# Performance work log

Hardware: AMD Instinct MI355X
Metric: run time of the kernel (lower is better)

## Reference

```python
import jax, jax.numpy as jnp
import numpy as np
from jax import lax

HEADS = 8

def rotate_every_two(x):
    x1 = x[..., ::2]
    x2 = x[..., 1::2]
    return jnp.stack([-x2, x1], axis=-1).reshape(x.shape)

def theta_shift(x, sin, cos):
    # x: (b,n,N,d); sin/cos: (N,d) broadcast over b,n
    return x * cos + rotate_every_two(x) * sin

def setup_inputs() -> dict:
    key = jax.random.key(0)
    ks = jax.random.split(key, 8)
    B, C, H, W = 8, 256, 64, 64
    hd = C // HEADS
    return {
        'x': jax.random.normal(ks[0], (B, C, H, W), jnp.float32),
        'sin': jax.random.normal(ks[1], (H * W, hd), jnp.float32),
        'cos': jax.random.normal(ks[2], (H * W, hd), jnp.float32),
        'w_qkvo': jax.random.normal(ks[3], (4 * C, C), jnp.float32) * 0.02,
        'b_qkvo': jnp.zeros((4 * C,), jnp.float32),
        'w_lepe': jax.random.normal(ks[4], (C, 1, 5, 5), jnp.float32) * 0.02,
        'b_lepe': jnp.zeros((C,), jnp.float32),
        'w_proj': jax.random.normal(ks[5], (C, C), jnp.float32) * 0.02,
        'b_proj': jnp.zeros((C,), jnp.float32),
    }

def reference(x, sin, cos, w_qkvo, b_qkvo, w_lepe, b_lepe, w_proj, b_proj):
    B, C, H, W = x.shape
    heads = HEADS
    hd = C // heads
    N = H * W
    scale = hd ** (-0.5)

    # 1x1 conv qkvo
    qkvo = jnp.einsum('bchw,oc->bohw', x, w_qkvo) + b_qkvo[None, :, None, None]
    qkv = qkvo[:, :3 * C]
    o = qkvo[:, 3 * C:]

    # depthwise 5x5 lepe on v channels
    v_img = qkv[:, 2 * C:]
    lepe = lax.conv_general_dilated(
        v_img, w_lepe, (1, 1), [(2, 2), (2, 2)],
        dimension_numbers=('NCHW', 'OIHW', 'NCHW'),
        feature_group_count=C) + b_lepe[None, :, None, None]

    # b (m n d) h w -> m b n (h w) d
    qkv_r = qkv.reshape(B, 3, heads, hd, N).transpose(1, 0, 2, 4, 3)
    q, k, v = qkv_r[0], qkv_r[1], qkv_r[2]  # (b,n,N,d)

    q = jax.nn.elu(q) + 1.0
    k = jax.nn.elu(k) + 1.0

    # z = q @ mean_k^T * scale -> (b,n,N,1)
    z = jnp.einsum('bnld,bnd->bnl', q, k.mean(axis=2))[..., None] * scale

    q = theta_shift(q, sin, cos)
    k = theta_shift(k, sin, cos)

    s = (scale / N) ** 0.5
    kv = jnp.einsum('bnld,bnle->bnde', k * s, v * s)  # (b,n,d,d)
    v_mean = v.mean(axis=2, keepdims=True)  # (b,n,1,d)

    res = jnp.einsum('bnld,bnde->bnle', q, kv) * (1.0 + 1.0 / (z + 1e-6)) - z * v_mean

    # b n (h w) d -> b (n d) h w
    res = res.transpose(0, 1, 3, 2).reshape(B, C, H, W)
    res = res + lepe

    out = jnp.einsum('bchw,oc->bohw', res * o, w_proj) + b_proj[None, :, None, None]
    return out
```

## Files before the change

### kernel.cpp

```cpp
#include <hip/hip_runtime.h>
#include <hip/hip_bf16.h>

typedef unsigned short u16;
typedef unsigned int u32;
typedef short bf16x8 __attribute__((ext_vector_type(8)));
typedef float f32x4 __attribute__((ext_vector_type(4)));
typedef u32 u32x4 __attribute__((ext_vector_type(4)));

#define N_TOK 4096
#define C_DIM 256
#define HEADS 8
#define HD 32
#define SCALE_F 0.17677669529663687f

__device__ inline u16 f2bf(float f) {
    u32 u = __float_as_uint(f);
    u += 0x7fffu + ((u >> 16) & 1u);
    return (u16)(u >> 16);
}
__device__ inline float b2f(u16 h) { return __uint_as_float((u32)h << 16); }
__device__ inline float bf_lo(u32 u) { return __uint_as_float(u << 16); }
__device__ inline float bf_hi(u32 u) { return __uint_as_float(u & 0xffff0000u); }

__device__ inline void gload16(const void* g, void* l) {
    __builtin_amdgcn_global_load_lds((const __attribute__((address_space(1))) u32*)g,
                                     (__attribute__((address_space(3))) u32*)l, 16, 0, 0);
}

__global__ __launch_bounds__(256) void stage1(const float* __restrict__ x, const float* __restrict__ w1,
                                              const float* __restrict__ w2, const float* __restrict__ s,
                                              const float* __restrict__ c, u16* __restrict__ xT,
                                              u16* __restrict__ o1, u16* __restrict__ o2, u32* __restrict__ scT) {
    __shared__ char smem[16896];
    int bx = blockIdx.x;
    int t = threadIdx.x;
    if (bx < 2048) {
        int lt = bx & 63, ct = (bx >> 6) & 3, b = bx >> 8;
        int l0 = lt * 64, c0 = ct * 64;
        const float* xb = x + ((size_t)b * C_DIM + c0) * N_TOK + l0;
        float* tl = (float*)smem;
#pragma unroll
        for (int i = 0; i < 4; ++i) {
            int id = i * 256 + t;
            int ci = id >> 4, lj = id & 15;
            f32x4 v = *(const f32x4*)(xb + (size_t)ci * N_TOK + lj * 4);
#pragma unroll
            for (int e = 0; e < 4; ++e) tl[(lj * 4 + e) * 65 + ci] = v[e];
        }
        __syncthreads();
#pragma unroll
        for (int j = 0; j < 2; ++j) {
            int id = j * 256 + t;
            int l = id >> 3, cg = id & 7;
            u16 o[8];
#pragma unroll
            for (int e = 0; e < 8; ++e) o[e] = f2bf(tl[l * 65 + cg * 8 + e]);
            uint4 u;
            u.x = (u32)o[0] | ((u32)o[1] << 16);
            u.y = (u32)o[2] | ((u32)o[3] << 16);
            u.z = (u32)o[4] | ((u32)o[5] << 16);
            u.w = (u32)o[6] | ((u32)o[7] << 16);
            *(uint4*)(xT + ((size_t)b * N_TOK + l0 + l) * C_DIM + c0 + cg * 8) = u;
        }
        return;
    }
    int px = bx - 2048;
    if (px < 1024) {
        int i = px * 256 + t;
        o1[i] = f2bf(w1[i]);
        if (i < 256 * 256) o2[i] = f2bf(w2[i]);
        return;
    }
    int l0 = (px - 1024) * 64;
    float (*ts)[33] = (float(*)[33])smem;
    float (*tc)[33] = (float(*)[33])(smem + 8448);
    int d = t & 31, r = t >> 5;
#pragma unroll
    for (int i = 0; i < 8; ++i) {
        ts[r + i * 8][d] = s[(size_t)(l0 + r + i * 8) * HD + d];
        tc[r + i * 8][d] = c[(size_t)(l0 + r + i * 8) * HD + d];
    }
    __syncthreads();
    int li = t & 63, dr = t >> 6;
#pragma unroll
    for (int i = 0; i < 8; ++i) {
        int dd = dr * 8 + i;
        scT[(size_t)dd * N_TOK + l0 + li] = (u32)f2bf(ts[li][dd]) | ((u32)f2bf(tc[li][dd]) << 16);
    }
}

__global__ __launch_bounds__(256) void gemm_proj(const u16* __restrict__ A, const u16* __restrict__ Bm,
                                                 const float* __restrict__ bias, float* __restrict__ C,
                                                 int M, int L, int K) {
    int bt = blockIdx.z;
    int m0 = blockIdx.y * 128;
    int l0 = blockIdx.x * 128;
    const u16* Bb = Bm + (size_t)bt * L * K;
    float* Cb = C + (size_t)bt * M * L;

    __shared__ u16 smem[17408];
    u16* As = smem;
    u16* Bs = smem + 8192;

    int t = threadIdx.x;
    int w = t >> 6, lane = t & 63;
    int wr = (w >> 1) * 64, wc = (w & 1) * 64;
    int fr = lane & 15, kg = lane >> 4;

    f32x4 acc[4][4] = {};

    for (int k0 = 0; k0 < K; k0 += 64) {
#pragma unroll
        for (int j = 0; j < 4; ++j) {
            int c = j * 256 + w * 64 + lane;
            int row = c >> 3, slot = c & 7;
            int gslot = slot ^ (row & 7);
            u16* abase = As + (size_t)(j * 256 + w * 64) * 8;
            u16* bbase = Bs + (size_t)(j * 256 + w * 64) * 8;
            gload16(A + (size_t)(m0 + row) * K + k0 + gslot * 8, abase);
            gload16(Bb + (size_t)(l0 + row) * K + k0 + gslot * 8, bbase);
        }
        __syncthreads();
#pragma unroll
        for (int kk = 0; kk < 2; ++kk) {
            bf16x8 af[4], bfr[4];
#pragma unroll
            for (int i = 0; i < 4; ++i) {
                int ra = wr + i * 16 + fr;
                int rb = wc + i * 16 + fr;
                af[i]  = *(const bf16x8*)(As + (size_t)ra * 64 + (size_t)((kk * 4 + kg) ^ (ra & 7)) * 8);
                bfr[i] = *(const bf16x8*)(Bs + (size_t)rb * 64 + (size_t)((kk * 4 + kg) ^ (rb & 7)) * 8);
            }
#pragma unroll
            for (int i = 0; i < 4; ++i)
#pragma unroll
                for (int jj = 0; jj < 4; ++jj)
                    acc[i][jj] = __builtin_amdgcn_mfma_f32_16x16x32_bf16(af[i], bfr[jj], acc[i][jj], 0, 0, 0);
        }
        __syncthreads();
    }

    int rg = (lane >> 4) * 4;
    float* Csf = (float*)smem;
#pragma unroll
    for (int half = 0; half < 2; ++half) {
        if ((w >> 1) == half) {
#pragma unroll
            for (int i = 0; i < 4; ++i)
#pragma unroll
                for (int jj = 0; jj < 4; ++jj) {
                    int col = wc + jj * 16 + fr;
#pragma unroll
                    for (int r = 0; r < 4; ++r) {
                        int row = i * 16 + rg + r;
                        Csf[row * 132 + col] = acc[i][jj][r] + bias[m0 + half * 64 + row];
                    }
                }
        }
        __syncthreads();
#pragma unroll
        for (int j = 0; j < 8; ++j) {
            int id = j * 256 + t;
            int row = id >> 5, c4 = id & 31;
            *(f32x4*)(Cb + (size_t)(m0 + half * 64 + row) * L + l0 + c4 * 4) =
                *(const f32x4*)(Csf + row * 132 + c4 * 4);
        }
        __syncthreads();
    }
}

__global__ __launch_bounds__(256) void stage2_kv(const u16* __restrict__ wbf, const float* __restrict__ bq,
                                                 const u16* __restrict__ xT, const u32* __restrict__ scT,
                                                 u16* __restrict__ v_glob, float* __restrict__ part_kv,
                                                 float* __restrict__ part_ks, float* __restrict__ part_vs) {
    int chunk = blockIdx.x & 15, bn = blockIdx.x >> 4;
    int b = bn >> 3, n = bn & 7;
    int T0 = chunk * 256;
    const u16* Bx = xT + ((size_t)b * N_TOK + T0) * C_DIM;

    __shared__ char smem[51200];
    u16* Bst = (u16*)smem;
    u16* Ast = (u16*)(smem + 32768);
    u16 (*ks_bf)[264] = (u16(*)[264])smem;
    u16 (*v_bf)[264]  = (u16(*)[264])(smem + 16896);
    float* red  = (float*)(smem + 33792);
    float* redk = (float*)(smem + 50176);
    float* redv = (float*)(smem + 50688);

    int t = threadIdx.x;
    int w = t >> 6, lane = t & 63;
    int fr = lane & 15, kg = lane >> 4;

    float bk[8], bv[8];
#pragma unroll
    for (int i = 0; i < 2; ++i)
#pragma unroll
        for (int r = 0; r < 4; ++r) {
            bk[i * 4 + r] = bq[256 + n * HD + i * 16 + kg * 4 + r];
            bv[i * 4 + r] = bq[512 + n * HD + i * 16 + kg * 4 + r];
        }

    f32x4 acc[4][4] = {};
    for (int k0 = 0; k0 < 256; k0 += 64) {
#pragma unroll
        for (int j = 0; j < 8; ++j) {
            int c = j * 256 + w * 64 + lane;
            int row = c >> 3, slot = c & 7;
            int gslot = slot ^ (row & 7);
            gload16(Bx + (size_t)row * C_DIM + k0 + gslot * 8, Bst + (size_t)(j * 256 + w * 64) * 8);
        }
#pragma unroll
        for (int j = 0; j < 2; ++j) {
            int c = j * 256 + w * 64 + lane;
            int row = c >> 3, slot = c & 7;
            int gslot = slot ^ (row & 7);
            int arow = (row < 32 ? 256 : 480) + n * HD + row;
            gload16(wbf + (size_t)arow * C_DIM + k0 + gslot * 8, Ast + (size_t)(j * 256 + w * 64) * 8);
        }
        __syncthreads();
#pragma unroll
        for (int kk = 0; kk < 2; ++kk) {
            bf16x8 af[4], bfr[4];
#pragma unroll
            for (int i = 0; i < 4; ++i) {
                int ra = i * 16 + fr;
                af[i] = *(const bf16x8*)(Ast + (size_t)ra * 64 + (size_t)((kk * 4 + kg) ^ (ra & 7)) * 8);
            }
#pragma unroll
            for (int jj = 0; jj < 4; ++jj) {
                int rb = w * 64 + jj * 16 + fr;
                bfr[jj] = *(const bf16x8*)(Bst + (size_t)rb * 64 + (size_t)((kk * 4 + kg) ^ (rb & 7)) * 8);
            }
#pragma unroll
            for (int i = 0; i < 4; ++i)
#pragma unroll
                for (int jj = 0; jj < 4; ++jj)
                    acc[i][jj] = __builtin_amdgcn_mfma_f32_16x16x32_bf16(af[i], bfr[jj], acc[i][jj], 0, 0, 0);
        }
        __syncthreads();
    }

    float kspart[8] = {}, vspart[8] = {};
#pragma unroll
    for (int i = 0; i < 2; ++i)
#pragma unroll
        for (int jj = 0; jj < 4; ++jj) {
            int tok = w * 64 + jj * 16 + fr;
            float k0v = acc[i][jj][0] + bk[i * 4 + 0];
            float k1v = acc[i][jj][1] + bk[i * 4 + 1];
            float k2v = acc[i][jj][2] + bk[i * 4 + 2];
            float k3v = acc[i][jj][3] + bk[i * 4 + 3];
            float e0 = k0v > 0.f ? k0v + 1.f : __expf(k0v);
            float e1 = k1v > 0.f ? k1v + 1.f : __expf(k1v);
            float e2 = k2v > 0.f ? k2v + 1.f : __expf(k2v);
            float e3 = k3v > 0.f ? k3v + 1.f : __expf(k3v);
            kspart[i * 4 + 0] += e0; kspart[i * 4 + 1] += e1;
            kspart[i * 4 + 2] += e2; kspart[i * 4 + 3] += e3;
            int d0 = i * 16 + kg * 4;
            u32 sA = scT[(size_t)(d0 + 0) * N_TOK + T0 + tok];
            u32 sB = scT[(size_t)(d0 + 1) * N_TOK + T0 + tok];
            u32 sC = scT[(size_t)(d0 + 2) * N_TOK + T0 + tok];
            u32 sD = scT[(size_t)(d0 + 3) * N_TOK + T0 + tok];
            ks_bf[d0 + 0][tok] = f2bf(e0 * bf_hi(sA) - e1 * bf_lo(sA));
            ks_bf[d0 + 1][tok] = f2bf(e1 * bf_hi(sB) + e0 * bf_lo(sB));
            ks_bf[d0 + 2][tok] = f2bf(e2 * bf_hi(sC) - e3 * bf_lo(sC));
            ks_bf[d0 + 3][tok] = f2bf(e3 * bf_hi(sD) + e2 * bf_lo(sD));
        }
#pragma unroll
    for (int i = 2; i < 4; ++i)
#pragma unroll
        for (int jj = 0; jj < 4; ++jj) {
            int tok = w * 64 + jj * 16 + fr;
#pragma unroll
            for (int r = 0; r < 4; ++r) {
                int vrow = (i - 2) * 16 + kg * 4 + r;
                float vv_ = acc[i][jj][r] + bv[(i - 2) * 4 + r];
                vspart[(i - 2) * 4 + r] += vv_;
                v_bf[vrow][tok] = f2bf(vv_);
            }
        }
#pragma unroll
    for (int m = 1; m < 16; m <<= 1) {
#pragma unroll
        for (int q = 0; q < 8; ++q) {
            kspart[q] += __shfl_xor(kspart[q], m);
            vspart[q] += __shfl_xor(vspart[q], m);
        }
    }
    if (fr == 0) {
#pragma unroll
        for (int q = 0; q < 8; ++q) {
            int row = (q >> 2) * 16 + kg * 4 + (q & 3);
            redk[w * 32 + row] = kspart[q];
            redv[w * 32 + row] = vspart[q];
        }
    }
    __syncthreads();

    f32x4 a2[2][2] = {};
#pragma unroll
    for (int kc = 0; kc < 2; ++kc) {
        int kcol = w * 64 + kc * 32 + kg * 8;
        bf16x8 af[2], bfv[2];
#pragma unroll
        for (int i = 0; i < 2; ++i) {
            af[i]  = *(const bf16x8*)&ks_bf[i * 16 + fr][kcol];
            bfv[i] = *(const bf16x8*)&v_bf[i * 16 + fr][kcol];
        }
#pragma unroll
        for (int i = 0; i < 2; ++i)
#pragma unroll
            for (int jj = 0; jj < 2; ++jj)
                a2[i][jj] = __builtin_amdgcn_mfma_f32_16x16x32_bf16(af[i], bfv[jj], a2[i][jj], 0, 0, 0);
    }

    {
        int row = t >> 3, tg = t & 7;
        u16* vg = v_glob + ((size_t)(b * C_DIM + n * HD + row)) * N_TOK + T0 + tg * 32;
#pragma unroll
        for (int q = 0; q < 4; ++q)
            *(uint4*)(vg + q * 8) = *(const uint4*)&v_bf[row][tg * 32 + q * 8];
    }
    if (t < 32) {
        float s = redk[t] + redk[32 + t] + redk[64 + t] + redk[96 + t];
        float sv = redv[t] + redv[32 + t] + redv[64 + t] + redv[96 + t];
        part_ks[((size_t)bn * 16 + chunk) * 32 + t] = s;
        part_vs[((size_t)bn * 16 + chunk) * 32 + t] = sv;
    }

#pragma unroll
    for (int i = 0; i < 2; ++i)
#pragma unroll
        for (int jj = 0; jj < 2; ++jj)
#pragma unroll
            for (int r = 0; r < 4; ++r) {
                int row = i * 16 + kg * 4 + r;
                int col = jj * 16 + fr;
                red[w * 1024 + row * 32 + col] = a2[i][jj][r];
            }
    __syncthreads();
    float* pkv = part_kv + ((size_t)bn * 16 + chunk) * 1024;
#pragma unroll
    for (int i = 0; i < 4; ++i) {
        int el = i * 256 + t;
        pkv[el] = red[el] + red[1024 + el] + red[2048 + el] + red[3072 + el];
    }
}

__global__ __launch_bounds__(256) void kvfinal_lepe(const float* __restrict__ part_kv, const float* __restrict__ part_ks,
                                                    const float* __restrict__ part_vs, const u16* __restrict__ v_glob,
                                                    const float* __restrict__ wl, const float* __restrict__ bl,
                                                    u16* __restrict__ kvT_bf, float* __restrict__ kmean,
                                                    float* __restrict__ vmean, u16* __restrict__ lepe) {
    __shared__ float wc5[25];
    int bx = blockIdx.x;
    int t = threadIdx.x;
    if (bx < 64) {
        int bn = bx;
        const float* p = part_kv + (size_t)bn * 16 * 1024;
        const float s2c = SCALE_F / (float)N_TOK;
#pragma unroll
        for (int i = 0; i < 4; ++i) {
            int sl = t + i * 256;
            float s = 0;
#pragma unroll
            for (int c = 0; c < 16; ++c) s += p[(size_t)c * 1024 + sl];
            float val = s * s2c;
            int d = sl >> 5, e = sl & 31;
            kvT_bf[(size_t)bn * 1024 + e * 32 + d] = f2bf(val);
        }
        if (t < 32) {
            float s = 0, sv = 0;
            for (int c = 0; c < 16; ++c) {
                s  += part_ks[((size_t)bn * 16 + c) * 32 + t];
                sv += part_vs[((size_t)bn * 16 + c) * 32 + t];
            }
            kmean[bn * 32 + t] = s * (1.f / (float)N_TOK);
            vmean[bn * 32 + t] = sv * (1.f / (float)N_TOK);
        }
        return;
    }
    int i2 = bx - 64;
    int c = i2 & 255, b = i2 >> 8;
    const u16* src = v_glob + ((size_t)(b * C_DIM + c)) * N_TOK;
    u16* dst = lepe + ((size_t)b * C_DIM + c) * N_TOK;
    if (t < 25) wc5[t] = wl[c * 25 + t];
    __syncthreads();

    int h = t >> 2, w0 = (t & 3) * 16;
    float bb = bl[c];
    float o16[16];
#pragma unroll
    for (int i = 0; i < 16; ++i) o16[i] = bb;

#pragma unroll
    for (int dh = 0; dh < 5; ++dh) {
        int gr = h + dh - 2;
        bool rowok = (gr >= 0) && (gr < 64);
        const u16* rp = src + (size_t)(rowok ? gr : 0) * 64 + w0 - 8;
        bf16x8 L0 = ((const bf16x8*)rp)[0];
        bf16x8 L1 = ((const bf16x8*)rp)[1];
        bf16x8 L2 = ((const bf16x8*)rp)[2];
        bf16x8 L3 = ((const bf16x8*)rp)[3];
        float rbuf[32];
#pragma unroll
        for (int j = 0; j < 32; ++j) {
            int col = w0 - 8 + j;
            u16 raw = (u16)(j < 8 ? L0[j] : j < 16 ? L1[j - 8] : j < 24 ? L2[j - 16] : L3[j - 24]);
            bool ok = rowok && (col >= 0) && (col < 64);
            rbuf[j] = ok ? b2f(raw) : 0.f;
        }
#pragma unroll
        for (int dw = 0; dw < 5; ++dw) {
            float wv_ = wc5[dh * 5 + dw];
#pragma unroll
            for (int ow = 0; ow < 16; ++ow)
                o16[ow] += rbuf[6 + dw + ow] * wv_;
        }
    }

    uint4 u0, u1;
    u0.x = (u32)f2bf(o16[0]) | ((u32)f2bf(o16[1]) << 16);
    u0.y = (u32)f2bf(o16[2]) | ((u32)f2bf(o16[3]) << 16);
    u0.z = (u32)f2bf(o16[4]) | ((u32)f2bf(o16[5]) << 16);
    u0.w = (u32)f2bf(o16[6]) | ((u32)f2bf(o16[7]) << 16);
    u1.x = (u32)f2bf(o16[8]) | ((u32)f2bf(o16[9]) << 16);
    u1.y = (u32)f2bf(o16[10]) | ((u32)f2bf(o16[11]) << 16);
    u1.z = (u32)f2bf(o16[12]) | ((u32)f2bf(o16[13]) << 16);
    u1.w = (u32)f2bf(o16[14]) | ((u32)f2bf(o16[15]) << 16);
    *(uint4*)(dst + h * 64 + w0) = u0;
    *(uint4*)(dst + h * 64 + w0 + 8) = u1;
}

__global__ __launch_bounds__(256) void attn_epilogue(const u16* __restrict__ wbf, const float* __restrict__ bq,
                                                     const u16* __restrict__ xT, const u32* __restrict__ scT,
                                                     const u16* __restrict__ kvT_bf, const float* __restrict__ kmean,
                                                     const float* __restrict__ vmean, const u16* __restrict__ lepe,
                                                     u16* __restrict__ resnT) {
    int lt = blockIdx.x, bn = blockIdx.y;
    int b = bn >> 3, n = bn & 7;
    int T0 = lt * 256;
    const u16* lp = lepe + ((size_t)b * C_DIM + n * HD) * N_TOK;
    const u16* Bx = xT + ((size_t)b * N_TOK + T0) * C_DIM;

    __shared__ char smem[64256];
    u16* qA    = (u16*)smem;
    u16* o_lds = (u16*)(smem + 20480);
    u16* Rt    = (u16*)(smem + 40960);
    u16* kvb   = (u16*)(smem + 61440);
    float* kml = (float*)(smem + 64000);
    float* vml = (float*)(smem + 64128);
    u16* Bst = (u16*)smem;
    u16* Ast = (u16*)(smem + 32768);

    int t = threadIdx.x;
    int w = t >> 6, lane = t & 63;
    int fr = lane & 15, kg = lane >> 4;

    if (t < 128) {
        int e = t >> 2, d0 = (t & 3) * 8;
        *(uint4*)(kvb + e * 40 + d0) = *(const uint4*)(kvT_bf + (size_t)bn * 1024 + e * 32 + d0);
    }
    if (t < 32) { kml[t] = kmean[bn * 32 + t]; vml[t] = vmean[bn * 32 + t]; }

    f32x4 acc[4][4] = {};
    for (int k0 = 0; k0 < 256; k0 += 64) {
#pragma unroll
        for (int j = 0; j < 8; ++j) {
            int c = j * 256 + w * 64 + lane;
            int row = c >> 3, slot = c & 7;
            int gslot = slot ^ (row & 7);
            gload16(Bx + (size_t)row * C_DIM + k0 + gslot * 8, Bst + (size_t)(j * 256 + w * 64) * 8);
        }
#pragma unroll
        for (int j = 0; j < 2; ++j) {
            int c = j * 256 + w * 64 + lane;
            int row = c >> 3, slot = c & 7;
            int gslot = slot ^ (row & 7);
            int arow = (row < 32 ? n * HD : 736 + n * HD) + row;
            gload16(wbf + (size_t)arow * C_DIM + k0 + gslot * 8, Ast + (size_t)(j * 256 + w * 64) * 8);
        }
        __syncthreads();
#pragma unroll
        for (int kk = 0; kk < 2; ++kk) {
            bf16x8 af[4], bfr[4];
#pragma unroll
            for (int i = 0; i < 4; ++i) {
                int ra = i * 16 + fr;
                af[i] = *(const bf16x8*)(Ast + (size_t)ra * 64 + (size_t)((kk * 4 + kg) ^ (ra & 7)) * 8);
            }
#pragma unroll
            for (int jj = 0; jj < 4; ++jj) {
                int rb = w * 64 + jj * 16 + fr;
                bfr[jj] = *(const bf16x8*)(Bst + (size_t)rb * 64 + (size_t)((kk * 4 + kg) ^ (rb & 7)) * 8);
            }
#pragma unroll
            for (int i = 0; i < 4; ++i)
#pragma unroll
                for (int jj = 0; jj < 4; ++jj)
                    acc[i][jj] = __builtin_amdgcn_mfma_f32_16x16x32_bf16(af[i], bfr[jj], acc[i][jj], 0, 0, 0);
        }
        __syncthreads();
    }
    int rg = kg * 4;
#pragma unroll
    for (int i = 0; i < 4; ++i)
#pragma unroll
        for (int jj = 0; jj < 4; ++jj) {
            int tok = w * 64 + jj * 16 + fr;
#pragma unroll
            for (int r = 0; r < 4; ++r) {
                int qorow = i * 16 + rg + r;
                int brow = (qorow < 32 ? n * HD : 736 + n * HD) + qorow;
                u16 val = f2bf(acc[i][jj][r] + bq[brow]);
                if (qorow < 32) qA[tok * 40 + qorow] = val;
                else            o_lds[tok * 40 + qorow - 32] = val;
            }
        }
    __syncthreads();

    int token = T0 + t;
    float qv[32];
    float z = 0.f;
#pragma unroll
    for (int j = 0; j < 4; ++j) {
        bf16x8 q8 = *(const bf16x8*)(qA + t * 40 + j * 8);
#pragma unroll
        for (int e = 0; e < 8; ++e) {
            float x_ = b2f((u16)q8[e]);
            float e_ = x_ > 0.f ? x_ + 1.f : __expf(x_);
            qv[j * 8 + e] = e_;
            z += e_ * kml[j * 8 + e];
        }
    }
    z *= SCALE_F;
#pragma unroll
    for (int p = 0; p < 16; ++p) {
        u32 sc0 = scT[(size_t)(2 * p) * N_TOK + token];
        u32 sc1 = scT[(size_t)(2 * p + 1) * N_TOK + token];
        float se = bf_lo(sc0), ce = bf_hi(sc0);
        float so = bf_lo(sc1), co = bf_hi(sc1);
        float a = qv[2 * p], bb = qv[2 * p + 1];
        qv[2 * p]     = a * ce - bb * se;
        qv[2 * p + 1] = bb * co + a * so;
    }
    float mult = 1.f + 1.f / (z + 1e-6f);
#pragma unroll
    for (int j4 = 0; j4 < 4; ++j4) {
        uint4 u;
        u.x = (u32)f2bf(qv[8 * j4 + 0]) | ((u32)f2bf(qv[8 * j4 + 1]) << 16);
        u.y = (u32)f2bf(qv[8 * j4 + 2]) | ((u32)f2bf(qv[8 * j4 + 3]) << 16);
        u.z = (u32)f2bf(qv[8 * j4 + 4]) | ((u32)f2bf(qv[8 * j4 + 5]) << 16);
        u.w = (u32)f2bf(qv[8 * j4 + 6]) | ((u32)f2bf(qv[8 * j4 + 7]) << 16);
        *(uint4*)(qA + t * 40 + j4 * 8) = u;
    }
    __syncthreads();

    {
        bf16x8 af[4], bfr[2];
#pragma unroll
        for (int i = 0; i < 4; ++i)
            af[i] = *(const bf16x8*)(qA + (size_t)(w * 64 + i * 16 + fr) * 40 + kg * 8);
#pragma unroll
        for (int jj = 0; jj < 2; ++jj)
            bfr[jj] = *(const bf16x8*)(kvb + (jj * 16 + fr) * 40 + kg * 8);

        u16* Rw = Rt + w * 2560;
        f32x4 zero = {0.f, 0.f, 0.f, 0.f};
#pragma unroll
        for (int i = 0; i < 4; ++i)
#pragma unroll
            for (int jj = 0; jj < 2; ++jj) {
                f32x4 a2 = __builtin_amdgcn_mfma_f32_16x16x32_bf16(af[i], bfr[jj], zero, 0, 0, 0);
#pragma unroll
                for (int r = 0; r < 4; ++r)
                    Rw[(i * 16 + kg * 4 + r) * 40 + jj * 16 + fr] = f2bf(a2[r]);
            }
    }
    __syncthreads();

    float res[32], ovv[32];
#pragma unroll
    for (int j = 0; j < 4; ++j) {
        bf16x8 r8 = *(const bf16x8*)(Rt + w * 2560 + lane * 40 + j * 8);
        bf16x8 o8 = *(const bf16x8*)(o_lds + t * 40 + j * 8);
#pragma unroll
        for (int e = 0; e < 8; ++e) {
            res[j * 8 + e] = b2f((u16)r8[e]);
            ovv[j * 8 + e] = b2f((u16)o8[e]);
        }
    }

    u16* dst0 = resnT + ((size_t)b * N_TOK + token) * C_DIM + n * HD;
#pragma unroll
    for (int g = 0; g < 4; ++g) {
        float vv[8];
#pragma unroll
        for (int e2 = 0; e2 < 8; ++e2) {
            int ee = g * 8 + e2;
            float lx = b2f(lp[(size_t)ee * N_TOK + token]);
            float rx = res[ee] * mult - z * vml[ee];
            vv[e2] = (rx + lx) * ovv[ee];
        }
        uint4 u;
        u.x = (u32)f2bf(vv[0]) | ((u32)f2bf(vv[1]) << 16);
        u.y = (u32)f2bf(vv[2]) | ((u32)f2bf(vv[3]) << 16);
        u.z = (u32)f2bf(vv[4]) | ((u32)f2bf(vv[5]) << 16);
        u.w = (u32)f2bf(vv[6]) | ((u32)f2bf(vv[7]) << 16);
        ((uint4*)(dst0 + g * 8))[0] = u;
    }
}

extern "C" void kernel_launch(void* const* d_in, const int* in_sizes, int n_in,
                              void* d_out, int out_size, void* d_ws, size_t ws_size,
                              hipStream_t stream) {
    const float* x      = (const float*)d_in[0];
    const float* sinp   = (const float*)d_in[1];
    const float* cosp   = (const float*)d_in[2];
    const float* w_qkvo = (const float*)d_in[3];
    const float* b_qkvo = (const float*)d_in[4];
    const float* w_lepe = (const float*)d_in[5];
    const float* b_lepe = (const float*)d_in[6];
    const float* w_proj = (const float*)d_in[7];
    const float* b_proj = (const float*)d_in[8];

    char* ws = (char*)d_ws;
    size_t off = 0;
    auto alloc = [&](size_t bytes) { size_t o = off; off = (off + bytes + 255) & ~(size_t)255; return o; };
    u16*   wbf     = (u16*)(ws + alloc((size_t)1024 * 256 * 2));
    u16*   wpbf    = (u16*)(ws + alloc((size_t)256 * 256 * 2));
    u16*   xT      = (u16*)(ws + alloc((size_t)8 * 4096 * 256 * 2));
    u16*   v_glob  = (u16*)(ws + alloc((size_t)8 * 256 * 4096 * 2));
    u16*   lepe    = (u16*)(ws + alloc((size_t)8 * 256 * 4096 * 2));
    u16*   resnT   = (u16*)(ws + alloc((size_t)8 * 4096 * 256 * 2));
    float* part_kv = (float*)(ws + alloc((size_t)64 * 16 * 1024 * 4));
    float* part_ks = (float*)(ws + alloc((size_t)64 * 16 * 32 * 4));
    float* part_vs = (float*)(ws + alloc((size_t)64 * 16 * 32 * 4));
    u16*   kvT_bf  = (u16*)(ws + alloc((size_t)64 * 1024 * 2));
    float* kmean   = (float*)(ws + alloc((size_t)64 * 32 * 4));
    float* vmean   = (float*)(ws + alloc((size_t)64 * 32 * 4));
    u32*   scT     = (u32*)(ws + alloc((size_t)32 * 4096 * 4));
    if (off > ws_size) return;

    stage1<<<dim3(3136), dim3(256), 0, stream>>>(x, w_qkvo, w_proj, sinp, cosp, xT, wbf, wpbf, scT);
    stage2_kv<<<dim3(1024), dim3(256), 0, stream>>>(wbf, b_qkvo, xT, scT, v_glob, part_kv, part_ks, part_vs);
    kvfinal_lepe<<<dim3(2112), dim3(256), 0, stream>>>(part_kv, part_ks, part_vs, v_glob, w_lepe, b_lepe,
                                                       kvT_bf, kmean, vmean, lepe);
    attn_epilogue<<<dim3(16, 64), dim3(256), 0, stream>>>(wbf, b_qkvo, xT, scT, kvT_bf, kmean, vmean, lepe, resnT);
    gemm_proj<<<dim3(32, 2, 8), dim3(256), 0, stream>>>(wpbf, resnT, b_proj, (float*)d_out, 256, 4096, 256);
}
```

Measured before the change: 92.75 us.

## Double-buffer LDS staging in stage2_kv and attn_epilogue GEMM loops

Both projection GEMM loops now use two LDS buffers, so the global-to-LDS loads for the next K-slice are issued before the MFMAs on the current slice run. This hides memory latency behind compute. In attn_epilogue the loads of kv, kmean and vmean move after the GEMM, since the enlarged staging area overlaps their LDS region. The cost is LDS growing to 80 KB per block, which can lower the number of resident blocks per CU.

```diff
diff --git a/kernel.cpp b/kernel.cpp
--- a/kernel.cpp
+++ b/kernel.cpp
@@ -178,9 +178,7 @@
     int T0 = chunk * 256;
     const u16* Bx = xT + ((size_t)b * N_TOK + T0) * C_DIM;
 
-    __shared__ char smem[51200];
-    u16* Bst = (u16*)smem;
-    u16* Ast = (u16*)(smem + 32768);
+    __shared__ char smem[81920];
     u16 (*ks_bf)[264] = (u16(*)[264])smem;
     u16 (*v_bf)[264]  = (u16(*)[264])(smem + 16896);
     float* red  = (float*)(smem + 33792);
@@ -200,36 +198,45 @@
             bv[i * 4 + r] = bq[512 + n * HD + i * 16 + kg * 4 + r];
         }
 
-    f32x4 acc[4][4] = {};
-    for (int k0 = 0; k0 < 256; k0 += 64) {
+    auto STAGE = [&](int buf, int k0) {
+        u16* Bd = (u16*)smem + buf * 16384;
+        u16* Ad = (u16*)(smem + 65536) + buf * 4096;
 #pragma unroll
         for (int j = 0; j < 8; ++j) {
-            int c = j * 256 + w * 64 + lane;
-            int row = c >> 3, slot = c & 7;
+            int cc = j * 256 + w * 64 + lane;
+            int row = cc >> 3, slot = cc & 7;
             int gslot = slot ^ (row & 7);
-            gload16(Bx + (size_t)row * C_DIM + k0 + gslot * 8, Bst + (size_t)(j * 256 + w * 64) * 8);
+            gload16(Bx + (size_t)row * C_DIM + k0 + gslot * 8, Bd + (size_t)(j * 256 + w * 64) * 8);
         }
 #pragma unroll
         for (int j = 0; j < 2; ++j) {
-            int c = j * 256 + w * 64 + lane;
-            int row = c >> 3, slot = c & 7;
+            int cc = j * 256 + w * 64 + lane;
+            int row = cc >> 3, slot = cc & 7;
             int gslot = slot ^ (row & 7);
             int arow = (row < 32 ? 256 : 480) + n * HD + row;
-            gload16(wbf + (size_t)arow * C_DIM + k0 + gslot * 8, Ast + (size_t)(j * 256 + w * 64) * 8);
-        }
-        __syncthreads();
+            gload16(wbf + (size_t)arow * C_DIM + k0 + gslot * 8, Ad + (size_t)(j * 256 + w * 64) * 8);
+        }
+    };
+
+    f32x4 acc[4][4] = {};
+    STAGE(0, 0);
+    __syncthreads();
+    for (int step = 0; step < 4; ++step) {
+        if (step < 3) STAGE((step + 1) & 1, (step + 1) * 64);
+        u16* Bc = (u16*)smem + (step & 1) * 16384;
+        u16* Ac = (u16*)(smem + 65536) + (step & 1) * 4096;
 #pragma unroll
         for (int kk = 0; kk < 2; ++kk) {
             bf16x8 af[4], bfr[4];
 #pragma unroll
             for (int i = 0; i < 4; ++i) {
                 int ra = i * 16 + fr;
-                af[i] = *(const bf16x8*)(Ast + (size_t)ra * 64 + (size_t)((kk * 4 + kg) ^ (ra & 7)) * 8);
+                af[i] = *(const bf16x8*)(Ac + (size_t)ra * 64 + (size_t)((kk * 4 + kg) ^ (ra & 7)) * 8);
             }
 #pragma unroll
             for (int jj = 0; jj < 4; ++jj) {
                 int rb = w * 64 + jj * 16 + fr;
-                bfr[jj] = *(const bf16x8*)(Bst + (size_t)rb * 64 + (size_t)((kk * 4 + kg) ^ (rb & 7)) * 8);
+                bfr[jj] = *(const bf16x8*)(Bc + (size_t)rb * 64 + (size_t)((kk * 4 + kg) ^ (rb & 7)) * 8);
             }
 #pragma unroll
             for (int i = 0; i < 4; ++i)
@@ -443,65 +450,72 @@
     const u16* lp = lepe + ((size_t)b * C_DIM + n * HD) * N_TOK;
     const u16* Bx = xT + ((size_t)b * N_TOK + T0) * C_DIM;
 
-    __shared__ char smem[64256];
+    __shared__ char smem[81920];
     u16* qA    = (u16*)smem;
     u16* o_lds = (u16*)(smem + 20480);
     u16* Rt    = (u16*)(smem + 40960);
     u16* kvb   = (u16*)(smem + 61440);
     float* kml = (float*)(smem + 64000);
     float* vml = (float*)(smem + 64128);
-    u16* Bst = (u16*)smem;
-    u16* Ast = (u16*)(smem + 32768);
 
     int t = threadIdx.x;
     int w = t >> 6, lane = t & 63;
     int fr = lane & 15, kg = lane >> 4;
 
+    auto STAGE = [&](int buf, int k0) {
+        u16* Bd = (u16*)smem + buf * 16384;
+        u16* Ad = (u16*)(smem + 65536) + buf * 4096;
+#pragma unroll
+        for (int j = 0; j < 8; ++j) {
+            int cc = j * 256 + w * 64 + lane;
+            int row = cc >> 3, slot = cc & 7;
+            int gslot = slot ^ (row & 7);
+            gload16(Bx + (size_t)row * C_DIM + k0 + gslot * 8, Bd + (size_t)(j * 256 + w * 64) * 8);
+        }
+#pragma unroll
+        for (int j = 0; j < 2; ++j) {
+            int cc = j * 256 + w * 64 + lane;
+            int row = cc >> 3, slot = cc & 7;
+            int gslot = slot ^ (row & 7);
+            int arow = (row < 32 ? n * HD : 736 + n * HD) + row;
+            gload16(wbf + (size_t)arow * C_DIM + k0 + gslot * 8, Ad + (size_t)(j * 256 + w * 64) * 8);
+        }
+    };
+
+    f32x4 acc[4][4] = {};
+    STAGE(0, 0);
+    __syncthreads();
+    for (int step = 0; step < 4; ++step) {
+        if (step < 3) STAGE((step + 1) & 1, (step + 1) * 64);
+        u16* Bc = (u16*)smem + (step & 1) * 16384;
+        u16* Ac = (u16*)(smem + 65536) + (step & 1) * 4096;
+#pragma unroll
+        for (int kk = 0; kk < 2; ++kk) {
+            bf16x8 af[4], bfr[4];
+#pragma unroll
+            for (int i = 0; i < 4; ++i) {
+                int ra = i * 16 + fr;
+                af[i] = *(const bf16x8*)(Ac + (size_t)ra * 64 + (size_t)((kk * 4 + kg) ^ (ra & 7)) * 8);
+            }
+#pragma unroll
+            for (int jj = 0; jj < 4; ++jj) {
+                int rb = w * 64 + jj * 16 + fr;
+                bfr[jj] = *(const bf16x8*)(Bc + (size_t)rb * 64 + (size_t)((kk * 4 + kg) ^ (rb & 7)) * 8);
+            }
+#pragma unroll
+            for (int i = 0; i < 4; ++i)
+#pragma unroll
+                for (int jj = 0; jj < 4; ++jj)
+                    acc[i][jj] = __builtin_amdgcn_mfma_f32_16x16x32_bf16(af[i], bfr[jj], acc[i][jj], 0, 0, 0);
+        }
+        __syncthreads();
+    }
+
     if (t < 128) {
         int e = t >> 2, d0 = (t & 3) * 8;
         *(uint4*)(kvb + e * 40 + d0) = *(const uint4*)(kvT_bf + (size_t)bn * 1024 + e * 32 + d0);
     }
     if (t < 32) { kml[t] = kmean[bn * 32 + t]; vml[t] = vmean[bn * 32 + t]; }
-
-    f32x4 acc[4][4] = {};
-    for (int k0 = 0; k0 < 256; k0 += 64) {
-#pragma unroll
-        for (int j = 0; j < 8; ++j) {
-            int c = j * 256 + w * 64 + lane;
-            int row = c >> 3, slot = c & 7;
-            int gslot = slot ^ (row & 7);
-            gload16(Bx + (size_t)row * C_DIM + k0 + gslot * 8, Bst + (size_t)(j * 256 + w * 64) * 8);
-        }
-#pragma unroll
-        for (int j = 0; j < 2; ++j) {
-            int c = j * 256 + w * 64 + lane;
-            int row = c >> 3, slot = c & 7;
-            int gslot = slot ^ (row & 7);
-            int arow = (row < 32 ? n * HD : 736 + n * HD) + row;
-            gload16(wbf + (size_t)arow * C_DIM + k0 + gslot * 8, Ast + (size_t)(j * 256 + w * 64) * 8);
-        }
-        __syncthreads();
-#pragma unroll
-        for (int kk = 0; kk < 2; ++kk) {
-            bf16x8 af[4], bfr[4];
-#pragma unroll
-            for (int i = 0; i < 4; ++i) {
-                int ra = i * 16 + fr;
-                af[i] = *(const bf16x8*)(Ast + (size_t)ra * 64 + (size_t)((kk * 4 + kg) ^ (ra & 7)) * 8);
-            }
-#pragma unroll
-            for (int jj = 0; jj < 4; ++jj) {
-                int rb = w * 64 + jj * 16 + fr;
-                bfr[jj] = *(const bf16x8*)(Bst + (size_t)rb * 64 + (size_t)((kk * 4 + kg) ^ (rb & 7)) * 8);
-            }
-#pragma unroll
-            for (int i = 0; i < 4; ++i)
-#pragma unroll
-                for (int jj = 0; jj < 4; ++jj)
-                    acc[i][jj] = __builtin_amdgcn_mfma_f32_16x16x32_bf16(af[i], bfr[jj], acc[i][jj], 0, 0, 0);
-        }
-        __syncthreads();
-    }
     int rg = kg * 4;
 #pragma unroll
     for (int i = 0; i < 4; ++i)
```

Result: slower. 95.29 us (+2.7%).

## Fuse depthwise lepe conv into attention epilogue via LDS tile

Applied to the files above, without the earlier changes.

Moves the 5x5 depthwise lepe convolution out of the separate kv-final kernel and into attn_epilogue. Each block computes the lepe values for its 4-row token tile and 32 head channels into shared memory. This removes the global lepe buffer write and re-read and leaves kv_final as a tiny 64-block kernel. In exchange, LDS use per block grows to about 80KB, which may lower occupancy, and the conv work now sits on the epilogue's critical path instead of running in parallel blocks.

```diff
diff --git a/kernel.cpp b/kernel.cpp
--- a/kernel.cpp
+++ b/kernel.cpp
@@ -204,15 +204,15 @@
     for (int k0 = 0; k0 < 256; k0 += 64) {
 #pragma unroll
         for (int j = 0; j < 8; ++j) {
-            int c = j * 256 + w * 64 + lane;
-            int row = c >> 3, slot = c & 7;
+            int cc = j * 256 + w * 64 + lane;
+            int row = cc >> 3, slot = cc & 7;
             int gslot = slot ^ (row & 7);
             gload16(Bx + (size_t)row * C_DIM + k0 + gslot * 8, Bst + (size_t)(j * 256 + w * 64) * 8);
         }
 #pragma unroll
         for (int j = 0; j < 2; ++j) {
-            int c = j * 256 + w * 64 + lane;
-            int row = c >> 3, slot = c & 7;
+            int cc = j * 256 + w * 64 + lane;
+            int row = cc >> 3, slot = cc & 7;
             int gslot = slot ^ (row & 7);
             int arow = (row < 32 ? 256 : 480) + n * HD + row;
             gload16(wbf + (size_t)arow * C_DIM + k0 + gslot * 8, Ast + (size_t)(j * 256 + w * 64) * 8);
@@ -347,109 +347,53 @@
     }
 }
 
-__global__ __launch_bounds__(256) void kvfinal_lepe(const float* __restrict__ part_kv, const float* __restrict__ part_ks,
-                                                    const float* __restrict__ part_vs, const u16* __restrict__ v_glob,
-                                                    const float* __restrict__ wl, const float* __restrict__ bl,
-                                                    u16* __restrict__ kvT_bf, float* __restrict__ kmean,
-                                                    float* __restrict__ vmean, u16* __restrict__ lepe) {
-    __shared__ float wc5[25];
-    int bx = blockIdx.x;
+__global__ __launch_bounds__(256) void kv_final(const float* __restrict__ part_kv, const float* __restrict__ part_ks,
+                                                const float* __restrict__ part_vs, u16* __restrict__ kvT_bf,
+                                                float* __restrict__ kmean, float* __restrict__ vmean) {
+    int bn = blockIdx.x;
     int t = threadIdx.x;
-    if (bx < 64) {
-        int bn = bx;
-        const float* p = part_kv + (size_t)bn * 16 * 1024;
-        const float s2c = SCALE_F / (float)N_TOK;
-#pragma unroll
-        for (int i = 0; i < 4; ++i) {
-            int sl = t + i * 256;
-            float s = 0;
-#pragma unroll
-            for (int c = 0; c < 16; ++c) s += p[(size_t)c * 1024 + sl];
-            float val = s * s2c;
-            int d = sl >> 5, e = sl & 31;
-            kvT_bf[(size_t)bn * 1024 + e * 32 + d] = f2bf(val);
-        }
-        if (t < 32) {
-            float s = 0, sv = 0;
-            for (int c = 0; c < 16; ++c) {
-                s  += part_ks[((size_t)bn * 16 + c) * 32 + t];
-                sv += part_vs[((size_t)bn * 16 + c) * 32 + t];
-            }
-            kmean[bn * 32 + t] = s * (1.f / (float)N_TOK);
-            vmean[bn * 32 + t] = sv * (1.f / (float)N_TOK);
-        }
-        return;
-    }
-    int i2 = bx - 64;
-    int c = i2 & 255, b = i2 >> 8;
-    const u16* src = v_glob + ((size_t)(b * C_DIM + c)) * N_TOK;
-    u16* dst = lepe + ((size_t)b * C_DIM + c) * N_TOK;
-    if (t < 25) wc5[t] = wl[c * 25 + t];
-    __syncthreads();
-
-    int h = t >> 2, w0 = (t & 3) * 16;
-    float bb = bl[c];
-    float o16[16];
-#pragma unroll
-    for (int i = 0; i < 16; ++i) o16[i] = bb;
-
-#pragma unroll
-    for (int dh = 0; dh < 5; ++dh) {
-        int gr = h + dh - 2;
-        bool rowok = (gr >= 0) && (gr < 64);
-        const u16* rp = src + (size_t)(rowok ? gr : 0) * 64 + w0 - 8;
-        bf16x8 L0 = ((const bf16x8*)rp)[0];
-        bf16x8 L1 = ((const bf16x8*)rp)[1];
-        bf16x8 L2 = ((const bf16x8*)rp)[2];
-        bf16x8 L3 = ((const bf16x8*)rp)[3];
-        float rbuf[32];
-#pragma unroll
-        for (int j = 0; j < 32; ++j) {
-            int col = w0 - 8 + j;
-            u16 raw = (u16)(j < 8 ? L0[j] : j < 16 ? L1[j - 8] : j < 24 ? L2[j - 16] : L3[j - 24]);
-            bool ok = rowok && (col >= 0) && (col < 64);
-            rbuf[j] = ok ? b2f(raw) : 0.f;
-        }
-#pragma unroll
-        for (int dw = 0; dw < 5; ++dw) {
-            float wv_ = wc5[dh * 5 + dw];
-#pragma unroll
-            for (int ow = 0; ow < 16; ++ow)
-                o16[ow] += rbuf[6 + dw + ow] * wv_;
-        }
-    }
-
-    uint4 u0, u1;
-    u0.x = (u32)f2bf(o16[0]) | ((u32)f2bf(o16[1]) << 16);
-    u0.y = (u32)f2bf(o16[2]) | ((u32)f2bf(o16[3]) << 16);
-    u0.z = (u32)f2bf(o16[4]) | ((u32)f2bf(o16[5]) << 16);
-    u0.w = (u32)f2bf(o16[6]) | ((u32)f2bf(o16[7]) << 16);
-    u1.x = (u32)f2bf(o16[8]) | ((u32)f2bf(o16[9]) << 16);
-    u1.y = (u32)f2bf(o16[10]) | ((u32)f2bf(o16[11]) << 16);
-    u1.z = (u32)f2bf(o16[12]) | ((u32)f2bf(o16[13]) << 16);
-    u1.w = (u32)f2bf(o16[14]) | ((u32)f2bf(o16[15]) << 16);
-    *(uint4*)(dst + h * 64 + w0) = u0;
-    *(uint4*)(dst + h * 64 + w0 + 8) = u1;
+    const float* p = part_kv + (size_t)bn * 16 * 1024;
+    const float s2c = SCALE_F / (float)N_TOK;
+#pragma unroll
+    for (int i = 0; i < 4; ++i) {
+        int sl = t + i * 256;
+        float s = 0;
+#pragma unroll
+        for (int c = 0; c < 16; ++c) s += p[(size_t)c * 1024 + sl];
+        float val = s * s2c;
+        int d = sl >> 5, e = sl & 31;
+        kvT_bf[(size_t)bn * 1024 + e * 32 + d] = f2bf(val);
+    }
+    if (t < 32) {
+        float s = 0, sv = 0;
+        for (int c = 0; c < 16; ++c) {
+            s  += part_ks[((size_t)bn * 16 + c) * 32 + t];
+            sv += part_vs[((size_t)bn * 16 + c) * 32 + t];
+        }
+        kmean[bn * 32 + t] = s * (1.f / (float)N_TOK);
+        vmean[bn * 32 + t] = sv * (1.f / (float)N_TOK);
+    }
 }
 
 __global__ __launch_bounds__(256) void attn_epilogue(const u16* __restrict__ wbf, const float* __restrict__ bq,
                                                      const u16* __restrict__ xT, const u32* __restrict__ scT,
                                                      const u16* __restrict__ kvT_bf, const float* __restrict__ kmean,
-                                                     const float* __restrict__ vmean, const u16* __restrict__ lepe,
+                                                     const float* __restrict__ vmean, const u16* __restrict__ v_glob,
+                                                     const float* __restrict__ wl, const float* __restrict__ bl,
                                                      u16* __restrict__ resnT) {
     int lt = blockIdx.x, bn = blockIdx.y;
     int b = bn >> 3, n = bn & 7;
     int T0 = lt * 256;
-    const u16* lp = lepe + ((size_t)b * C_DIM + n * HD) * N_TOK;
     const u16* Bx = xT + ((size_t)b * N_TOK + T0) * C_DIM;
 
-    __shared__ char smem[64256];
+    __shared__ char smem[80640];
     u16* qA    = (u16*)smem;
     u16* o_lds = (u16*)(smem + 20480);
     u16* Rt    = (u16*)(smem + 40960);
     u16* kvb   = (u16*)(smem + 61440);
     float* kml = (float*)(smem + 64000);
     float* vml = (float*)(smem + 64128);
+    u16* lepe_lds = (u16*)(smem + 64256);
     u16* Bst = (u16*)smem;
     u16* Ast = (u16*)(smem + 32768);
 
@@ -467,15 +411,15 @@
     for (int k0 = 0; k0 < 256; k0 += 64) {
 #pragma unroll
         for (int j = 0; j < 8; ++j) {
-            int c = j * 256 + w * 64 + lane;
-            int row = c >> 3, slot = c & 7;
+            int cc = j * 256 + w * 64 + lane;
+            int row = cc >> 3, slot = cc & 7;
             int gslot = slot ^ (row & 7);
             gload16(Bx + (size_t)row * C_DIM + k0 + gslot * 8, Bst + (size_t)(j * 256 + w * 64) * 8);
         }
 #pragma unroll
         for (int j = 0; j < 2; ++j) {
-            int c = j * 256 + w * 64 + lane;
-            int row = c >> 3, slot = c & 7;
+            int cc = j * 256 + w * 64 + lane;
+            int row = cc >> 3, slot = cc & 7;
             int gslot = slot ^ (row & 7);
             int arow = (row < 32 ? n * HD : 736 + n * HD) + row;
             gload16(wbf + (size_t)arow * C_DIM + k0 + gslot * 8, Ast + (size_t)(j * 256 + w * 64) * 8);
@@ -518,6 +462,56 @@
             }
         }
     __syncthreads();
+
+#pragma unroll
+    for (int q = 0; q < 2; ++q) {
+        int item = q * 256 + t;
+        int c = item >> 4, rr = (item >> 2) & 3, cg = item & 3;
+        int h = 4 * lt + rr;
+        int w0 = cg * 16;
+        const u16* vsrc = v_glob + ((size_t)(b * C_DIM + n * HD + c)) * N_TOK;
+        const float* wc5 = wl + (n * HD + c) * 25;
+        float bb = bl[n * HD + c];
+        float o16[16];
+#pragma unroll
+        for (int i = 0; i < 16; ++i) o16[i] = bb;
+#pragma unroll
+        for (int dh = 0; dh < 5; ++dh) {
+            int gr = h + dh - 2;
+            bool rowok = (gr >= 0) && (gr < 64);
+            const u16* rp = vsrc + (size_t)(rowok ? gr : 0) * 64 + w0 - 8;
+            bf16x8 L0 = ((const bf16x8*)rp)[0];
+            bf16x8 L1 = ((const bf16x8*)rp)[1];
+            bf16x8 L2 = ((const bf16x8*)rp)[2];
+            bf16x8 L3 = ((const bf16x8*)rp)[3];
+            float rbuf[32];
+#pragma unroll
+            for (int j = 0; j < 32; ++j) {
+                int col = w0 - 8 + j;
+                u16 raw = (u16)(j < 8 ? L0[j] : j < 16 ? L1[j - 8] : j < 24 ? L2[j - 16] : L3[j - 24]);
+                bool ok = rowok && (col >= 0) && (col < 64);
+                rbuf[j] = ok ? b2f(raw) : 0.f;
+            }
+#pragma unroll
+            for (int dw = 0; dw < 5; ++dw) {
+                float wv_ = wc5[dh * 5 + dw];
+#pragma unroll
+                for (int ow = 0; ow < 16; ++ow)
+                    o16[ow] += rbuf[6 + dw + ow] * wv_;
+            }
+        }
+        uint4 u0, u1;
+        u0.x = (u32)f2bf(o16[0]) | ((u32)f2bf(o16[1]) << 16);
+        u0.y = (u32)f2bf(o16[2]) | ((u32)f2bf(o16[3]) << 16);
+        u0.z = (u32)f2bf(o16[4]) | ((u32)f2bf(o16[5]) << 16);
+        u0.w = (u32)f2bf(o16[6]) | ((u32)f2bf(o16[7]) << 16);
+        u1.x = (u32)f2bf(o16[8]) | ((u32)f2bf(o16[9]) << 16);
+        u1.y = (u32)f2bf(o16[10]) | ((u32)f2bf(o16[11]) << 16);
+        u1.z = (u32)f2bf(o16[12]) | ((u32)f2bf(o16[13]) << 16);
+        u1.w = (u32)f2bf(o16[14]) | ((u32)f2bf(o16[15]) << 16);
+        *(uint4*)(lepe_lds + c * 256 + rr * 64 + w0) = u0;
+        *(uint4*)(lepe_lds + c * 256 + rr * 64 + w0 + 8) = u1;
+    }
 
     int token = T0 + t;
     float qv[32];
@@ -598,7 +592,7 @@
 #pragma unroll
         for (int e2 = 0; e2 < 8; ++e2) {
             int ee = g * 8 + e2;
-            float lx = b2f(lp[(size_t)ee * N_TOK + token]);
+            float lx = b2f(lepe_lds[ee * 256 + t]);
             float rx = res[ee] * mult - z * vml[ee];
             vv[e2] = (rx + lx) * ovv[ee];
         }
@@ -631,7 +625,6 @@
     u16*   wpbf    = (u16*)(ws + alloc((size_t)256 * 256 * 2));
     u16*   xT      = (u16*)(ws + alloc((size_t)8 * 4096 * 256 * 2));
     u16*   v_glob  = (u16*)(ws + alloc((size_t)8 * 256 * 4096 * 2));
-    u16*   lepe    = (u16*)(ws + alloc((size_t)8 * 256 * 4096 * 2));
     u16*   resnT   = (u16*)(ws + alloc((size_t)8 * 4096 * 256 * 2));
     float* part_kv = (float*)(ws + alloc((size_t)64 * 16 * 1024 * 4));
     float* part_ks = (float*)(ws + alloc((size_t)64 * 16 * 32 * 4));
@@ -644,8 +637,8 @@
 
     stage1<<<dim3(3136), dim3(256), 0, stream>>>(x, w_qkvo, w_proj, sinp, cosp, xT, wbf, wpbf, scT);
     stage2_kv<<<dim3(1024), dim3(256), 0, stream>>>(wbf, b_qkvo, xT, scT, v_glob, part_kv, part_ks, part_vs);
-    kvfinal_lepe<<<dim3(2112), dim3(256), 0, stream>>>(part_kv, part_ks, part_vs, v_glob, w_lepe, b_lepe,
-                                                       kvT_bf, kmean, vmean, lepe);
-    attn_epilogue<<<dim3(16, 64), dim3(256), 0, stream>>>(wbf, b_qkvo, xT, scT, kvT_bf, kmean, vmean, lepe, resnT);
+    kv_final<<<dim3(64), dim3(256), 0, stream>>>(part_kv, part_ks, part_vs, kvT_bf, kmean, vmean);
+    attn_epilogue<<<dim3(16, 64), dim3(256), 0, stream>>>(wbf, b_qkvo, xT, scT, kvT_bf, kmean, vmean,
+                                                          v_glob, w_lepe, b_lepe, resnT);
     gemm_proj<<<dim3(32, 2, 8), dim3(256), 0, stream>>>(wpbf, resnT, b_proj, (float*)d_out, 256, 4096, 256);
 }
```

Result: no change. 93.93 us (+1.3%).

## Restructure attention epilogue to keep o in registers and shrink LDS

Applied to the files above, without the earlier changes.

The attention epilogue now keeps the o-projection tile packed in registers and computes kv@q transposed, so the MFMA output layout matches the o tile. The final elementwise step (mult, z*vmean, lepe add, multiply by o) is fused right after the MFMA. Results are staged through LDS only for a coalesced row store. This cuts LDS from about 64KB to about 45KB, adds launch_bounds(256,3) for higher occupancy, and raises wave priority around the MFMA loop. In exchange, lepe reads become strided per-token gathers and register pressure may rise under the 3-block bound.

```diff
diff --git a/kernel.cpp b/kernel.cpp
--- a/kernel.cpp
+++ b/kernel.cpp
@@ -204,15 +204,15 @@
     for (int k0 = 0; k0 < 256; k0 += 64) {
 #pragma unroll
         for (int j = 0; j < 8; ++j) {
-            int c = j * 256 + w * 64 + lane;
-            int row = c >> 3, slot = c & 7;
+            int cc = j * 256 + w * 64 + lane;
+            int row = cc >> 3, slot = cc & 7;
             int gslot = slot ^ (row & 7);
             gload16(Bx + (size_t)row * C_DIM + k0 + gslot * 8, Bst + (size_t)(j * 256 + w * 64) * 8);
         }
 #pragma unroll
         for (int j = 0; j < 2; ++j) {
-            int c = j * 256 + w * 64 + lane;
-            int row = c >> 3, slot = c & 7;
+            int cc = j * 256 + w * 64 + lane;
+            int row = cc >> 3, slot = cc & 7;
             int gslot = slot ^ (row & 7);
             int arow = (row < 32 ? 256 : 480) + n * HD + row;
             gload16(wbf + (size_t)arow * C_DIM + k0 + gslot * 8, Ast + (size_t)(j * 256 + w * 64) * 8);
@@ -432,26 +432,27 @@
     *(uint4*)(dst + h * 64 + w0 + 8) = u1;
 }
 
-__global__ __launch_bounds__(256) void attn_epilogue(const u16* __restrict__ wbf, const float* __restrict__ bq,
-                                                     const u16* __restrict__ xT, const u32* __restrict__ scT,
-                                                     const u16* __restrict__ kvT_bf, const float* __restrict__ kmean,
-                                                     const float* __restrict__ vmean, const u16* __restrict__ lepe,
-                                                     u16* __restrict__ resnT) {
+__global__ __launch_bounds__(256, 3) void attn_epilogue(const u16* __restrict__ wbf, const float* __restrict__ bq,
+                                                        const u16* __restrict__ xT, const u32* __restrict__ scT,
+                                                        const u16* __restrict__ kvT_bf, const float* __restrict__ kmean,
+                                                        const float* __restrict__ vmean, const u16* __restrict__ lepe,
+                                                        u16* __restrict__ resnT) {
     int lt = blockIdx.x, bn = blockIdx.y;
     int b = bn >> 3, n = bn & 7;
     int T0 = lt * 256;
+    const u16* Bx = xT + ((size_t)b * N_TOK + T0) * C_DIM;
     const u16* lp = lepe + ((size_t)b * C_DIM + n * HD) * N_TOK;
-    const u16* Bx = xT + ((size_t)b * N_TOK + T0) * C_DIM;
-
-    __shared__ char smem[64256];
-    u16* qA    = (u16*)smem;
-    u16* o_lds = (u16*)(smem + 20480);
-    u16* Rt    = (u16*)(smem + 40960);
-    u16* kvb   = (u16*)(smem + 61440);
-    float* kml = (float*)(smem + 64000);
-    float* vml = (float*)(smem + 64128);
+
+    __shared__ char smem[45824];
     u16* Bst = (u16*)smem;
     u16* Ast = (u16*)(smem + 32768);
+    u16* qA  = (u16*)smem;
+    u16* vvb = (u16*)(smem + 20480);
+    u16* kvb = (u16*)(smem + 40960);
+    float* multL = (float*)(smem + 43520);
+    float* zL    = (float*)(smem + 44544);
+    float* kml   = (float*)(smem + 45568);
+    float* vml   = (float*)(smem + 45696);
 
     int t = threadIdx.x;
     int w = t >> 6, lane = t & 63;
@@ -463,24 +464,34 @@
     }
     if (t < 32) { kml[t] = kmean[bn * 32 + t]; vml[t] = vmean[bn * 32 + t]; }
 
+    float bkq[8], bko[8];
+#pragma unroll
+    for (int i = 0; i < 2; ++i)
+#pragma unroll
+        for (int r = 0; r < 4; ++r) {
+            bkq[i * 4 + r] = bq[n * HD + i * 16 + kg * 4 + r];
+            bko[i * 4 + r] = bq[768 + n * HD + i * 16 + kg * 4 + r];
+        }
+
     f32x4 acc[4][4] = {};
     for (int k0 = 0; k0 < 256; k0 += 64) {
 #pragma unroll
         for (int j = 0; j < 8; ++j) {
-            int c = j * 256 + w * 64 + lane;
-            int row = c >> 3, slot = c & 7;
+            int cc = j * 256 + w * 64 + lane;
+            int row = cc >> 3, slot = cc & 7;
             int gslot = slot ^ (row & 7);
             gload16(Bx + (size_t)row * C_DIM + k0 + gslot * 8, Bst + (size_t)(j * 256 + w * 64) * 8);
         }
 #pragma unroll
         for (int j = 0; j < 2; ++j) {
-            int c = j * 256 + w * 64 + lane;
-            int row = c >> 3, slot = c & 7;
+            int cc = j * 256 + w * 64 + lane;
+            int row = cc >> 3, slot = cc & 7;
             int gslot = slot ^ (row & 7);
             int arow = (row < 32 ? n * HD : 736 + n * HD) + row;
             gload16(wbf + (size_t)arow * C_DIM + k0 + gslot * 8, Ast + (size_t)(j * 256 + w * 64) * 8);
         }
         __syncthreads();
+        __builtin_amdgcn_s_setprio(1);
 #pragma unroll
         for (int kk = 0; kk < 2; ++kk) {
             bf16x8 af[4], bfr[4];
@@ -500,22 +511,24 @@
                 for (int jj = 0; jj < 4; ++jj)
                     acc[i][jj] = __builtin_amdgcn_mfma_f32_16x16x32_bf16(af[i], bfr[jj], acc[i][jj], 0, 0, 0);
         }
-        __syncthreads();
-    }
-    int rg = kg * 4;
-#pragma unroll
-    for (int i = 0; i < 4; ++i)
+        __builtin_amdgcn_s_setprio(0);
+        __syncthreads();
+    }
+
+    u32 o_pk[2][4][2];
+#pragma unroll
+    for (int i = 0; i < 2; ++i)
 #pragma unroll
         for (int jj = 0; jj < 4; ++jj) {
             int tok = w * 64 + jj * 16 + fr;
-#pragma unroll
-            for (int r = 0; r < 4; ++r) {
-                int qorow = i * 16 + rg + r;
-                int brow = (qorow < 32 ? n * HD : 736 + n * HD) + qorow;
-                u16 val = f2bf(acc[i][jj][r] + bq[brow]);
-                if (qorow < 32) qA[tok * 40 + qorow] = val;
-                else            o_lds[tok * 40 + qorow - 32] = val;
-            }
+            uint2 qp;
+            qp.x = (u32)f2bf(acc[i][jj][0] + bkq[i * 4 + 0]) | ((u32)f2bf(acc[i][jj][1] + bkq[i * 4 + 1]) << 16);
+            qp.y = (u32)f2bf(acc[i][jj][2] + bkq[i * 4 + 2]) | ((u32)f2bf(acc[i][jj][3] + bkq[i * 4 + 3]) << 16);
+            *(uint2*)(qA + tok * 40 + i * 16 + kg * 4) = qp;
+            o_pk[i][jj][0] = (u32)f2bf(acc[2 + i][jj][0] + bko[i * 4 + 0]) |
+                             ((u32)f2bf(acc[2 + i][jj][1] + bko[i * 4 + 1]) << 16);
+            o_pk[i][jj][1] = (u32)f2bf(acc[2 + i][jj][2] + bko[i * 4 + 2]) |
+                             ((u32)f2bf(acc[2 + i][jj][3] + bko[i * 4 + 3]) << 16);
         }
     __syncthreads();
 
@@ -544,7 +557,8 @@
         qv[2 * p]     = a * ce - bb * se;
         qv[2 * p + 1] = bb * co + a * so;
     }
-    float mult = 1.f + 1.f / (z + 1e-6f);
+    multL[t] = 1.f + 1.f / (z + 1e-6f);
+    zL[t] = z;
 #pragma unroll
     for (int j4 = 0; j4 < 4; ++j4) {
         uint4 u;
@@ -557,58 +571,48 @@
     __syncthreads();
 
     {
-        bf16x8 af[4], bfr[2];
-#pragma unroll
-        for (int i = 0; i < 4; ++i)
-            af[i] = *(const bf16x8*)(qA + (size_t)(w * 64 + i * 16 + fr) * 40 + kg * 8);
-#pragma unroll
-        for (int jj = 0; jj < 2; ++jj)
-            bfr[jj] = *(const bf16x8*)(kvb + (jj * 16 + fr) * 40 + kg * 8);
-
-        u16* Rw = Rt + w * 2560;
+        bf16x8 akv[2], bq8[4];
+#pragma unroll
+        for (int i2 = 0; i2 < 2; ++i2)
+            akv[i2] = *(const bf16x8*)(kvb + (i2 * 16 + fr) * 40 + kg * 8);
+#pragma unroll
+        for (int jj = 0; jj < 4; ++jj)
+            bq8[jj] = *(const bf16x8*)(qA + (size_t)(w * 64 + jj * 16 + fr) * 40 + kg * 8);
+
         f32x4 zero = {0.f, 0.f, 0.f, 0.f};
 #pragma unroll
-        for (int i = 0; i < 4; ++i)
-#pragma unroll
-            for (int jj = 0; jj < 2; ++jj) {
-                f32x4 a2 = __builtin_amdgcn_mfma_f32_16x16x32_bf16(af[i], bfr[jj], zero, 0, 0, 0);
-#pragma unroll
-                for (int r = 0; r < 4; ++r)
-                    Rw[(i * 16 + kg * 4 + r) * 40 + jj * 16 + fr] = f2bf(a2[r]);
+        for (int i2 = 0; i2 < 2; ++i2)
+#pragma unroll
+            for (int jj = 0; jj < 4; ++jj) {
+                f32x4 a2 = __builtin_amdgcn_mfma_f32_16x16x32_bf16(akv[i2], bq8[jj], zero, 0, 0, 0);
+                int tokloc = w * 64 + jj * 16 + fr;
+                float mult = multL[tokloc];
+                float zz = zL[tokloc];
+                u16 ovv[4];
+                ovv[0] = (u16)(o_pk[i2][jj][0] & 0xffff);
+                ovv[1] = (u16)(o_pk[i2][jj][0] >> 16);
+                ovv[2] = (u16)(o_pk[i2][jj][1] & 0xffff);
+                ovv[3] = (u16)(o_pk[i2][jj][1] >> 16);
+                u16 vvout[4];
+#pragma unroll
+                for (int r = 0; r < 4; ++r) {
+                    int e = i2 * 16 + kg * 4 + r;
+                    float lx = b2f(lp[(size_t)e * N_TOK + T0 + tokloc]);
+                    float vvf = (a2[r] * mult - zz * vml[e] + lx) * b2f(ovv[r]);
+                    vvout[r] = f2bf(vvf);
+                }
+                uint2 pk;
+                pk.x = (u32)vvout[0] | ((u32)vvout[1] << 16);
+                pk.y = (u32)vvout[2] | ((u32)vvout[3] << 16);
+                *(uint2*)(vvb + tokloc * 40 + i2 * 16 + kg * 4) = pk;
             }
     }
     __syncthreads();
 
-    float res[32], ovv[32];
-#pragma unroll
-    for (int j = 0; j < 4; ++j) {
-        bf16x8 r8 = *(const bf16x8*)(Rt + w * 2560 + lane * 40 + j * 8);
-        bf16x8 o8 = *(const bf16x8*)(o_lds + t * 40 + j * 8);
-#pragma unroll
-        for (int e = 0; e < 8; ++e) {
-            res[j * 8 + e] = b2f((u16)r8[e]);
-            ovv[j * 8 + e] = b2f((u16)o8[e]);
-        }
-    }
-
     u16* dst0 = resnT + ((size_t)b * N_TOK + token) * C_DIM + n * HD;
 #pragma unroll
-    for (int g = 0; g < 4; ++g) {
-        float vv[8];
-#pragma unroll
-        for (int e2 = 0; e2 < 8; ++e2) {
-            int ee = g * 8 + e2;
-            float lx = b2f(lp[(size_t)ee * N_TOK + token]);
-            float rx = res[ee] * mult - z * vml[ee];
-            vv[e2] = (rx + lx) * ovv[ee];
-        }
-        uint4 u;
-        u.x = (u32)f2bf(vv[0]) | ((u32)f2bf(vv[1]) << 16);
-        u.y = (u32)f2bf(vv[2]) | ((u32)f2bf(vv[3]) << 16);
-        u.z = (u32)f2bf(vv[4]) | ((u32)f2bf(vv[5]) << 16);
-        u.w = (u32)f2bf(vv[6]) | ((u32)f2bf(vv[7]) << 16);
-        ((uint4*)(dst0 + g * 8))[0] = u;
-    }
+    for (int g = 0; g < 4; ++g)
+        ((uint4*)dst0)[g] = *(const uint4*)(vvb + t * 40 + g * 8);
 }
 
 extern "C" void kernel_launch(void* const* d_in, const int* in_sizes, int n_in,
```

Measured after the change: 100.5 us. +8.3%, slower.
